# Kernel optimization log

Measured on AMD Instinct MI355X. Metric: run time of the kernel, lower is better.

## Reference

```python
import jax, jax.numpy as jnp
import numpy as np

B, D, IN_F, OUT_F, BLOCK = 2, 1024, 4096, 4096, 128
N_BLOCKS = IN_F // BLOCK  # 32


def setup_inputs() -> dict:
    key = jax.random.key(0)
    k1, k2, k3 = jax.random.split(key, 3)
    inputs = jax.random.normal(k1, (B, D, IN_F), dtype=jnp.float32)
    # int8 quantized weight buffer: [n_blocks, block_size, out_features]
    weight = jax.random.randint(k2, (N_BLOCKS, BLOCK, OUT_F), -128, 128, dtype=jnp.int32).astype(jnp.int8)
    # per-block, per-output-channel scaler: [n_blocks, out_features]
    weight_scaler = (jax.random.uniform(k3, (N_BLOCKS, OUT_F), dtype=jnp.float32) * 0.01 + 0.001)
    return {"inputs": inputs, "weight": weight, "weight_scaler": weight_scaler}


def reference(inputs, weight, weight_scaler):
    # Faithful port of WeightOnlyBlockwiseQuantizedLinear.blockwise_jax_kernel
    # (default path: symmetric quantization, zero_point is None).
    weight = weight.astype(jnp.int8)
    block_size = weight.shape[1]
    b, d, in_f = inputs.shape
    # [b, d, n_blocks s, block_size c]
    x = inputs.reshape(b, d, in_f // block_size, block_size)
    # per-block int8 matmul (promoted to float32 by x): [b, d, s, z]
    out = jnp.einsum("scz,bdsc->bdsz", weight, x)
    # apply per-block scaler and reduce over blocks: [b, d, z]
    out = jnp.einsum("bdsz,sz->bdz", out, weight_scaler)
    return out
```

## Files before the change

kernel.cpp:

```cpp
#include <hip/hip_runtime.h>
#include <hip/hip_bf16.h>


#define MDIM 2048
#define NDIM 4096
#define KDIM 4096
#define NBLK 32
#define BM 128
#define BN 128
#define BK 64

typedef __attribute__((ext_vector_type(8))) short bf16x8;
typedef __attribute__((ext_vector_type(4))) float f32x4;
typedef __attribute__((ext_vector_type(8))) unsigned short u16x8;

__device__ __forceinline__ unsigned short f2bf(float f) {
  unsigned u = __float_as_uint(f);
  u += 0x7fffu + ((u >> 16) & 1u);
  return (unsigned short)(u >> 16);
}

__device__ __forceinline__ void gl_lds16(const void* g, void* l) {
  __builtin_amdgcn_global_load_lds(
      (const __attribute__((address_space(1))) unsigned int*)g,
      (__attribute__((address_space(3))) unsigned int*)l,
      16, 0, 0);
}

__global__ void prep_a_kernel(const float* __restrict__ x,
                              unsigned short* __restrict__ ab) {
  int i = blockIdx.x * blockDim.x + threadIdx.x;
  const float4 v = reinterpret_cast<const float4*>(x)[i];
  ushort4 hv;
  hv.x = f2bf(v.x); hv.y = f2bf(v.y); hv.z = f2bf(v.z); hv.w = f2bf(v.w);
  reinterpret_cast<ushort4*>(ab)[i] = hv;
}

__global__ void prep_b_kernel(const int* __restrict__ w,
                              const float* __restrict__ scaler,
                              unsigned short* __restrict__ bt) {
  __shared__ __align__(16) unsigned short tile[64][72];
  const int t = threadIdx.x;
  const int k0 = blockIdx.y * 64;
  const int n0 = blockIdx.x * 64;
  const int s = k0 >> 7;
  {
    const int kl = t >> 2;
    const int nb = t & 3;
    const int nbase = n0 + nb * 16;
    const int4* src = reinterpret_cast<const int4*>(w + (size_t)(k0 + kl) * NDIM + nbase);
    const float4* scv = reinterpret_cast<const float4*>(scaler + (size_t)s * NDIM + nbase);
#pragma unroll
    for (int q = 0; q < 4; ++q) {
      const int4 v = src[q];
      const float4 sc = scv[q];
      tile[nb * 16 + q * 4 + 0][kl] = f2bf((float)v.x * sc.x);
      tile[nb * 16 + q * 4 + 1][kl] = f2bf((float)v.y * sc.y);
      tile[nb * 16 + q * 4 + 2][kl] = f2bf((float)v.z * sc.z);
      tile[nb * 16 + q * 4 + 3][kl] = f2bf((float)v.w * sc.w);
    }
  }
  __syncthreads();
  {
    const int nl = t >> 2;
#pragma unroll
    for (int q = 0; q < 2; ++q) {
      const int ch = (t & 3) * 2 + q;
      u16x8 v = *reinterpret_cast<const u16x8*>(&tile[nl][ch * 8]);
      *reinterpret_cast<u16x8*>(bt + (size_t)(n0 + nl) * KDIM + k0 + ch * 8) = v;
    }
  }
}

__global__ __launch_bounds__(256, 2)
void gemm_kernel(const unsigned short* __restrict__ ab,
                 const unsigned short* __restrict__ bt,
                 float* __restrict__ out) {
  __shared__ __align__(16) unsigned short lds_a[BM * BK];
  __shared__ __align__(16) unsigned short lds_b[BN * BK];

  const int t = threadIdx.x;
  const int lane = t & 63;
  const int wid = t >> 6;
  const int wm = wid >> 1;
  const int wn = wid & 1;
  const int lane15 = lane & 15;
  const int laneq = lane >> 4;
  const int swz = (lane & 7) << 4;

  const unsigned flat = blockIdx.x;
  const unsigned swzb = (flat & 7u) * 64u + (flat >> 3);
  const int ntile = swzb & 31;
  const int mtile = swzb >> 5;
  const int m0 = mtile * BM;
  const int n0 = ntile * BN;

  const int srow = t >> 3;
  const int sslot = (t & 7) ^ (srow & 7);
  const char* ga = (const char*)ab + ((size_t)(m0 + srow) * KDIM) * 2 + sslot * 16;
  const char* gb = (const char*)bt + ((size_t)(n0 + srow) * KDIM) * 2 + sslot * 16;
  const size_t rowstep = (size_t)32 * KDIM * 2;

  char* const la = (char*)lds_a;
  char* const lb = (char*)lds_b;
  const int ldst = wid * 8 * 128;

  int offA[4], offB[4];
#pragma unroll
  for (int i = 0; i < 4; ++i) {
    offA[i] = (wm * 64 + i * 16 + lane15) * 128 + laneq * 16;
    offB[i] = (wn * 64 + i * 16 + lane15) * 128 + laneq * 16;
  }

  const f32x4 fzero = {0.f, 0.f, 0.f, 0.f};
  f32x4 acc[4][4];
#pragma unroll
  for (int m = 0; m < 4; ++m)
#pragma unroll
    for (int n = 0; n < 4; ++n) acc[m][n] = fzero;

  for (int kt = 0; kt < KDIM / BK; ++kt) {
    const size_t koff = (size_t)kt * (BK * 2);
#pragma unroll
    for (int j = 0; j < 4; ++j) {
      gl_lds16(ga + koff + j * rowstep, la + ldst + j * 32 * 128);
      gl_lds16(gb + koff + j * rowstep, lb + ldst + j * 32 * 128);
    }
    __syncthreads();
#pragma unroll
    for (int tt = 0; tt < 2; ++tt) {
      bf16x8 af[4], bf[4];
#pragma unroll
      for (int i = 0; i < 4; ++i) {
        af[i] = *(const bf16x8*)(la + ((offA[i] + tt * 64) ^ swz));
        bf[i] = *(const bf16x8*)(lb + ((offB[i] + tt * 64) ^ swz));
      }
#pragma unroll
      for (int m = 0; m < 4; ++m)
#pragma unroll
        for (int n = 0; n < 4; ++n)
          acc[m][n] = __builtin_amdgcn_mfma_f32_16x16x32_bf16(af[m], bf[n], acc[m][n], 0, 0, 0);
    }
    __syncthreads();
  }

#pragma unroll
  for (int m = 0; m < 4; ++m)
#pragma unroll
    for (int r = 0; r < 4; ++r) {
      const int row = m0 + wm * 64 + m * 16 + laneq * 4 + r;
      float* op = out + (size_t)row * NDIM + n0 + wn * 64 + lane15;
#pragma unroll
      for (int n = 0; n < 4; ++n) op[n * 16] = acc[m][n][r];
    }
}

__global__ void fallback_kernel(const float* __restrict__ x,
                                const int* __restrict__ w,
                                const float* __restrict__ scaler,
                                float* __restrict__ out) {
  const int n = blockIdx.x * 256 + threadIdx.x;
  const int m = blockIdx.y;
  float acc = 0.f;
  for (int s = 0; s < NBLK; ++s) {
    float p = 0.f;
    const float* xr = x + (size_t)m * KDIM + s * 128;
    const int* wr = w + (size_t)s * 128 * NDIM + n;
#pragma unroll 8
    for (int c = 0; c < 128; ++c) p += xr[c] * (float)wr[(size_t)c * NDIM];
    acc += p * scaler[s * NDIM + n];
  }
  out[(size_t)m * NDIM + n] = acc;
}

extern "C" void kernel_launch(void* const* d_in, const int* in_sizes, int n_in,
                              void* d_out, int out_size, void* d_ws, size_t ws_size,
                              hipStream_t stream) {
  (void)in_sizes; (void)n_in; (void)out_size;
  const float* x = (const float*)d_in[0];
  const int* w = (const int*)d_in[1];
  const float* sc = (const float*)d_in[2];
  float* out = (float*)d_out;

  const size_t need = (size_t)51 * 1024 * 1024;
  if (ws_size >= need) {
    unsigned short* ab = (unsigned short*)d_ws;
    unsigned short* bt = ab + (size_t)MDIM * KDIM;
    prep_a_kernel<<<(MDIM * KDIM / 4) / 256, 256, 0, stream>>>(x, ab);
    prep_b_kernel<<<dim3(NDIM / 64, KDIM / 64), 256, 0, stream>>>(w, sc, bt);
    gemm_kernel<<<(MDIM / BM) * (NDIM / BN), 256, 0, stream>>>(ab, bt, out);
  } else {
    fallback_kernel<<<dim3(NDIM / 256, MDIM), 256, 0, stream>>>(x, w, sc, out);
  }
}
```

Baseline: 209.3 us.

## Double-buffer 128x256 GEMM tiles with 8 waves and ping-pong MFMA scheduling

Widens the GEMM tile to 128x256 with 512 threads and double-buffers the LDS stages, so global-to-LDS loads for step k+2 overlap MFMA work. The k-loop is split into quads of MFMAs separated by barriers with setprio, to interleave LDS reads and math across waves. The prep_b transpose tile gets an XOR swizzle to cut LDS bank conflicts. The larger LDS footprint lowers per-CU occupancy, and the many barriers add sync cost.

```diff
diff --git a/kernel.cpp b/kernel.cpp
--- a/kernel.cpp
+++ b/kernel.cpp
@@ -7,8 +7,9 @@
 #define KDIM 4096
 #define NBLK 32
 #define BM 128
-#define BN 128
+#define BN 256
 #define BK 64
+#define NT (KDIM / BK)
 
 typedef __attribute__((ext_vector_type(8))) short bf16x8;
 typedef __attribute__((ext_vector_type(4))) float f32x4;
@@ -54,44 +55,49 @@
     for (int q = 0; q < 4; ++q) {
       const int4 v = src[q];
       const float4 sc = scv[q];
-      tile[nb * 16 + q * 4 + 0][kl] = f2bf((float)v.x * sc.x);
-      tile[nb * 16 + q * 4 + 1][kl] = f2bf((float)v.y * sc.y);
-      tile[nb * 16 + q * 4 + 2][kl] = f2bf((float)v.z * sc.z);
-      tile[nb * 16 + q * 4 + 3][kl] = f2bf((float)v.w * sc.w);
+      const int rbase = nb * 16 + q * 4;
+      const int swzr = ((rbase >> 3) & 7) << 3;
+      const int ckl = kl ^ swzr;
+      tile[rbase + 0][ckl] = f2bf((float)v.x * sc.x);
+      tile[rbase + 1][ckl] = f2bf((float)v.y * sc.y);
+      tile[rbase + 2][ckl] = f2bf((float)v.z * sc.z);
+      tile[rbase + 3][ckl] = f2bf((float)v.w * sc.w);
     }
   }
   __syncthreads();
   {
     const int nl = t >> 2;
+    const int swzn = (nl >> 3) & 7;
 #pragma unroll
     for (int q = 0; q < 2; ++q) {
       const int ch = (t & 3) * 2 + q;
-      u16x8 v = *reinterpret_cast<const u16x8*>(&tile[nl][ch * 8]);
+      u16x8 v = *reinterpret_cast<const u16x8*>(&tile[nl][(ch ^ swzn) * 8]);
       *reinterpret_cast<u16x8*>(bt + (size_t)(n0 + nl) * KDIM + k0 + ch * 8) = v;
     }
   }
 }
 
-__global__ __launch_bounds__(256, 2)
+#define MFMA_BF16 __builtin_amdgcn_mfma_f32_16x16x32_bf16
+
+__global__ __launch_bounds__(512, 2)
 void gemm_kernel(const unsigned short* __restrict__ ab,
                  const unsigned short* __restrict__ bt,
                  float* __restrict__ out) {
-  __shared__ __align__(16) unsigned short lds_a[BM * BK];
-  __shared__ __align__(16) unsigned short lds_b[BN * BK];
+  __shared__ __align__(16) char lds[98304];
 
   const int t = threadIdx.x;
   const int lane = t & 63;
   const int wid = t >> 6;
-  const int wm = wid >> 1;
-  const int wn = wid & 1;
+  const int wm = wid >> 2;
+  const int wn = wid & 3;
   const int lane15 = lane & 15;
   const int laneq = lane >> 4;
   const int swz = (lane & 7) << 4;
 
   const unsigned flat = blockIdx.x;
-  const unsigned swzb = (flat & 7u) * 64u + (flat >> 3);
-  const int ntile = swzb & 31;
-  const int mtile = swzb >> 5;
+  const unsigned swzb = (flat & 7u) * 32u + (flat >> 3);
+  const int ntile = swzb & 15;
+  const int mtile = swzb >> 4;
   const int m0 = mtile * BM;
   const int n0 = ntile * BN;
 
@@ -99,11 +105,22 @@
   const int sslot = (t & 7) ^ (srow & 7);
   const char* ga = (const char*)ab + ((size_t)(m0 + srow) * KDIM) * 2 + sslot * 16;
   const char* gb = (const char*)bt + ((size_t)(n0 + srow) * KDIM) * 2 + sslot * 16;
-  const size_t rowstep = (size_t)32 * KDIM * 2;
-
-  char* const la = (char*)lds_a;
-  char* const lb = (char*)lds_b;
-  const int ldst = wid * 8 * 128;
+  const size_t rstep = (size_t)64 * KDIM * 2;
+
+  char* const lA0 = lds + (size_t)wid * 1024;
+  char* const lB0 = lds + 32768 + (size_t)wid * 1024;
+
+#define STAGE(kt, c) do {                                   \
+    const size_t ko_ = (size_t)(kt) * (BK * 2);             \
+    char* a_ = lA0 + (c) * 16384;                           \
+    char* b_ = lB0 + (c) * 32768;                           \
+    gl_lds16(ga + ko_,             a_);                     \
+    gl_lds16(ga + ko_ + rstep,     a_ + 8192);              \
+    gl_lds16(gb + ko_,             b_);                     \
+    gl_lds16(gb + ko_ + rstep,     b_ + 8192);              \
+    gl_lds16(gb + ko_ + 2 * rstep, b_ + 16384);             \
+    gl_lds16(gb + ko_ + 3 * rstep, b_ + 24576);             \
+  } while (0)
 
   int offA[4], offB[4];
 #pragma unroll
@@ -119,29 +136,63 @@
 #pragma unroll
     for (int n = 0; n < 4; ++n) acc[m][n] = fzero;
 
-  for (int kt = 0; kt < KDIM / BK; ++kt) {
-    const size_t koff = (size_t)kt * (BK * 2);
-#pragma unroll
-    for (int j = 0; j < 4; ++j) {
-      gl_lds16(ga + koff + j * rowstep, la + ldst + j * 32 * 128);
-      gl_lds16(gb + koff + j * rowstep, lb + ldst + j * 32 * 128);
-    }
-    __syncthreads();
-#pragma unroll
-    for (int tt = 0; tt < 2; ++tt) {
-      bf16x8 af[4], bf[4];
-#pragma unroll
-      for (int i = 0; i < 4; ++i) {
-        af[i] = *(const bf16x8*)(la + ((offA[i] + tt * 64) ^ swz));
-        bf[i] = *(const bf16x8*)(lb + ((offB[i] + tt * 64) ^ swz));
-      }
-#pragma unroll
-      for (int m = 0; m < 4; ++m)
-#pragma unroll
-        for (int n = 0; n < 4; ++n)
-          acc[m][n] = __builtin_amdgcn_mfma_f32_16x16x32_bf16(af[m], bf[n], acc[m][n], 0, 0, 0);
-    }
-    __syncthreads();
+  STAGE(0, 0);
+  STAGE(1, 1);
+  asm volatile("s_waitcnt vmcnt(6)" ::: "memory");
+  __builtin_amdgcn_s_barrier();
+
+#define LDA(m, base) do {                                             \
+    af[m][0] = *(const bf16x8*)((base) + ((offA[m]) ^ swz));          \
+    af[m][1] = *(const bf16x8*)((base) + ((offA[m] + 64) ^ swz));     \
+  } while (0)
+#define LDB(n, base) do {                                             \
+    bfr[n][0] = *(const bf16x8*)((base) + ((offB[n]) ^ swz));         \
+    bfr[n][1] = *(const bf16x8*)((base) + ((offB[n] + 64) ^ swz));    \
+  } while (0)
+#define QUAD(mA, mB, nA, nB) do {                                     \
+    __builtin_amdgcn_s_setprio(1);                                    \
+    acc[mA][nA] = MFMA_BF16(af[mA][0], bfr[nA][0], acc[mA][nA], 0, 0, 0); \
+    acc[mA][nB] = MFMA_BF16(af[mA][0], bfr[nB][0], acc[mA][nB], 0, 0, 0); \
+    acc[mB][nA] = MFMA_BF16(af[mB][0], bfr[nA][0], acc[mB][nA], 0, 0, 0); \
+    acc[mB][nB] = MFMA_BF16(af[mB][0], bfr[nB][0], acc[mB][nB], 0, 0, 0); \
+    acc[mA][nA] = MFMA_BF16(af[mA][1], bfr[nA][1], acc[mA][nA], 0, 0, 0); \
+    acc[mA][nB] = MFMA_BF16(af[mA][1], bfr[nB][1], acc[mA][nB], 0, 0, 0); \
+    acc[mB][nA] = MFMA_BF16(af[mB][1], bfr[nA][1], acc[mB][nA], 0, 0, 0); \
+    acc[mB][nB] = MFMA_BF16(af[mB][1], bfr[nB][1], acc[mB][nB], 0, 0, 0); \
+    __builtin_amdgcn_s_setprio(0);                                    \
+  } while (0)
+
+#pragma unroll 2
+  for (int t2 = 0; t2 < NT; ++t2) {
+    const int c = t2 & 1;
+    const char* lac = lds + c * 16384;
+    const char* lbc = lds + 32768 + c * 32768;
+    bf16x8 af[4][2], bfr[4][2];
+
+    LDA(0, lac); LDA(1, lac); LDB(0, lbc); LDB(1, lbc);
+    __builtin_amdgcn_s_barrier();
+    QUAD(0, 1, 0, 1);
+    __builtin_amdgcn_s_barrier();
+
+    LDB(2, lbc); LDB(3, lbc);
+    __builtin_amdgcn_s_barrier();
+    QUAD(0, 1, 2, 3);
+    __builtin_amdgcn_s_barrier();
+
+    LDA(2, lac); LDA(3, lac);
+    __builtin_amdgcn_s_barrier();
+    QUAD(2, 3, 2, 3);
+    __builtin_amdgcn_s_barrier();
+    __builtin_amdgcn_sched_barrier(0);
+
+    if (t2 + 2 < NT) STAGE(t2 + 2, c);
+    QUAD(2, 3, 0, 1);
+    if (t2 + 2 < NT) {
+      asm volatile("s_waitcnt vmcnt(6)" ::: "memory");
+    } else {
+      asm volatile("s_waitcnt vmcnt(0)" ::: "memory");
+    }
+    __builtin_amdgcn_s_barrier();
   }
 
 #pragma unroll
@@ -153,6 +204,10 @@
 #pragma unroll
       for (int n = 0; n < 4; ++n) op[n * 16] = acc[m][n][r];
     }
+#undef STAGE
+#undef LDA
+#undef LDB
+#undef QUAD
 }
 
 __global__ void fallback_kernel(const float* __restrict__ x,
@@ -188,7 +243,7 @@
     unsigned short* bt = ab + (size_t)MDIM * KDIM;
     prep_a_kernel<<<(MDIM * KDIM / 4) / 256, 256, 0, stream>>>(x, ab);
     prep_b_kernel<<<dim3(NDIM / 64, KDIM / 64), 256, 0, stream>>>(w, sc, bt);
-    gemm_kernel<<<(MDIM / BM) * (NDIM / BN), 256, 0, stream>>>(ab, bt, out);
+    gemm_kernel<<<(MDIM / BM) * (NDIM / BN), 512, 0, stream>>>(ab, bt, out);
   } else {
     fallback_kernel<<<dim3(NDIM / 256, MDIM), 256, 0, stream>>>(x, w, sc, out);
   }
```

Result: faster. 203.8 us (-2.6%).

## Fuse activation bf16 conversion into GEMM and rewrite weight prep without LDS

Applied to the files above, without the earlier changes.

Removes the separate prep_a kernel: the GEMM now loads fp32 activations directly, converts them to bf16 in registers with v_cvt_pk_bf16_f32, and writes them into swizzled LDS. The weight prep kernel is rewritten to transpose 8x8 sub-blocks in registers over 128x128 tiles, with no shared-memory tile. Occupancy hints are raised. This drops one launch and the round trip of the bf16 activation buffer through memory, but each GEMM tile now re-reads fp32 activations (twice the bytes) and converts them again, with synchronous loads in place of async global-to-LDS.

```diff
diff --git a/kernel.cpp b/kernel.cpp
--- a/kernel.cpp
+++ b/kernel.cpp
@@ -9,10 +9,12 @@
 #define BM 128
 #define BN 128
 #define BK 64
+#define NT (KDIM / BK)
 
 typedef __attribute__((ext_vector_type(8))) short bf16x8;
 typedef __attribute__((ext_vector_type(4))) float f32x4;
 typedef __attribute__((ext_vector_type(8))) unsigned short u16x8;
+typedef __attribute__((ext_vector_type(4))) unsigned int u32x4;
 
 __device__ __forceinline__ unsigned short f2bf(float f) {
   unsigned u = __float_as_uint(f);
@@ -27,57 +29,45 @@
       16, 0, 0);
 }
 
-__global__ void prep_a_kernel(const float* __restrict__ x,
-                              unsigned short* __restrict__ ab) {
-  int i = blockIdx.x * blockDim.x + threadIdx.x;
-  const float4 v = reinterpret_cast<const float4*>(x)[i];
-  ushort4 hv;
-  hv.x = f2bf(v.x); hv.y = f2bf(v.y); hv.z = f2bf(v.z); hv.w = f2bf(v.w);
-  reinterpret_cast<ushort4*>(ab)[i] = hv;
-}
-
-__global__ void prep_b_kernel(const int* __restrict__ w,
-                              const float* __restrict__ scaler,
-                              unsigned short* __restrict__ bt) {
-  __shared__ __align__(16) unsigned short tile[64][72];
+__global__ __launch_bounds__(256, 4)
+void prep_b_kernel(const int* __restrict__ w,
+                   const float* __restrict__ scaler,
+                   unsigned short* __restrict__ bt) {
   const int t = threadIdx.x;
-  const int k0 = blockIdx.y * 64;
-  const int n0 = blockIdx.x * 64;
-  const int s = k0 >> 7;
+  const int n0 = blockIdx.x * 128;
+  const int k0 = blockIdx.y * 128;
+  const int s = blockIdx.y;
+  const int k8 = (t & 15) * 8;
+  const int n8 = (t >> 4) * 8;
+
+  float sc[8];
   {
-    const int kl = t >> 2;
-    const int nb = t & 3;
-    const int nbase = n0 + nb * 16;
-    const int4* src = reinterpret_cast<const int4*>(w + (size_t)(k0 + kl) * NDIM + nbase);
-    const float4* scv = reinterpret_cast<const float4*>(scaler + (size_t)s * NDIM + nbase);
-#pragma unroll
-    for (int q = 0; q < 4; ++q) {
-      const int4 v = src[q];
-      const float4 sc = scv[q];
-      tile[nb * 16 + q * 4 + 0][kl] = f2bf((float)v.x * sc.x);
-      tile[nb * 16 + q * 4 + 1][kl] = f2bf((float)v.y * sc.y);
-      tile[nb * 16 + q * 4 + 2][kl] = f2bf((float)v.z * sc.z);
-      tile[nb * 16 + q * 4 + 3][kl] = f2bf((float)v.w * sc.w);
-    }
-  }
-  __syncthreads();
-  {
-    const int nl = t >> 2;
-#pragma unroll
-    for (int q = 0; q < 2; ++q) {
-      const int ch = (t & 3) * 2 + q;
-      u16x8 v = *reinterpret_cast<const u16x8*>(&tile[nl][ch * 8]);
-      *reinterpret_cast<u16x8*>(bt + (size_t)(n0 + nl) * KDIM + k0 + ch * 8) = v;
-    }
-  }
-}
-
-__global__ __launch_bounds__(256, 2)
-void gemm_kernel(const unsigned short* __restrict__ ab,
+    const float4* scv = reinterpret_cast<const float4*>(scaler + (size_t)s * NDIM + n0 + n8);
+    const float4 s0 = scv[0], s1 = scv[1];
+    sc[0] = s0.x; sc[1] = s0.y; sc[2] = s0.z; sc[3] = s0.w;
+    sc[4] = s1.x; sc[5] = s1.y; sc[6] = s1.z; sc[7] = s1.w;
+  }
+  u16x8 outv[8];
+#pragma unroll
+  for (int r = 0; r < 8; ++r) {
+    const int4* src = reinterpret_cast<const int4*>(w + (size_t)(k0 + k8 + r) * NDIM + n0 + n8);
+    const int4 a = src[0], b = src[1];
+    const int v[8] = {a.x, a.y, a.z, a.w, b.x, b.y, b.z, b.w};
+#pragma unroll
+    for (int j = 0; j < 8; ++j) outv[j][r] = f2bf((float)v[j] * sc[j]);
+  }
+#pragma unroll
+  for (int j = 0; j < 8; ++j)
+    *reinterpret_cast<u16x8*>(bt + (size_t)(n0 + n8 + j) * KDIM + k0 + k8) = outv[j];
+}
+
+#define MFMA_BF16 __builtin_amdgcn_mfma_f32_16x16x32_bf16
+
+__global__ __launch_bounds__(256, 3)
+void gemm_kernel(const float* __restrict__ x,
                  const unsigned short* __restrict__ bt,
                  float* __restrict__ out) {
-  __shared__ __align__(16) unsigned short lds_a[BM * BK];
-  __shared__ __align__(16) unsigned short lds_b[BN * BK];
+  __shared__ __align__(16) char lds[32768];
 
   const int t = threadIdx.x;
   const int lane = t & 63;
@@ -95,15 +85,23 @@
   const int m0 = mtile * BM;
   const int n0 = ntile * BN;
 
+  char* const lA = lds;
+  char* const lB = lds + 16384;
+
+  const int arow = t >> 3;
+  const int achk = t & 7;
+  const float* gx = x + (size_t)(m0 + arow) * KDIM + achk * 8;
+  const int aswz = (arow & 7) << 4;
+  int aoff[4];
+#pragma unroll
+  for (int p = 0; p < 4; ++p)
+    aoff[p] = (((arow + p * 32) * 128) + achk * 16) ^ aswz;
+
   const int srow = t >> 3;
   const int sslot = (t & 7) ^ (srow & 7);
-  const char* ga = (const char*)ab + ((size_t)(m0 + srow) * KDIM) * 2 + sslot * 16;
   const char* gb = (const char*)bt + ((size_t)(n0 + srow) * KDIM) * 2 + sslot * 16;
-  const size_t rowstep = (size_t)32 * KDIM * 2;
-
-  char* const la = (char*)lds_a;
-  char* const lb = (char*)lds_b;
-  const int ldst = wid * 8 * 128;
+  const size_t rstepB = (size_t)32 * KDIM * 2;
+  char* const lbst = lB + wid * 1024;
 
   int offA[4], offB[4];
 #pragma unroll
@@ -119,27 +117,44 @@
 #pragma unroll
     for (int n = 0; n < 4; ++n) acc[m][n] = fzero;
 
-  for (int kt = 0; kt < KDIM / BK; ++kt) {
-    const size_t koff = (size_t)kt * (BK * 2);
-#pragma unroll
-    for (int j = 0; j < 4; ++j) {
-      gl_lds16(ga + koff + j * rowstep, la + ldst + j * 32 * 128);
-      gl_lds16(gb + koff + j * rowstep, lb + ldst + j * 32 * 128);
-    }
+  for (int kt = 0; kt < NT; ++kt) {
+    float4 va[4][2];
+#pragma unroll
+    for (int p = 0; p < 4; ++p) {
+      const float* src = gx + (size_t)p * 32 * KDIM + kt * 64;
+      va[p][0] = *reinterpret_cast<const float4*>(src);
+      va[p][1] = *reinterpret_cast<const float4*>(src + 4);
+    }
+#pragma unroll
+    for (int p = 0; p < 4; ++p) {
+      unsigned d0, d1, d2, d3;
+      asm("v_cvt_pk_bf16_f32 %0, %1, %2" : "=v"(d0) : "v"(va[p][0].x), "v"(va[p][0].y));
+      asm("v_cvt_pk_bf16_f32 %0, %1, %2" : "=v"(d1) : "v"(va[p][0].z), "v"(va[p][0].w));
+      asm("v_cvt_pk_bf16_f32 %0, %1, %2" : "=v"(d2) : "v"(va[p][1].x), "v"(va[p][1].y));
+      asm("v_cvt_pk_bf16_f32 %0, %1, %2" : "=v"(d3) : "v"(va[p][1].z), "v"(va[p][1].w));
+      u32x4 wv = {d0, d1, d2, d3};
+      *reinterpret_cast<u32x4*>(lA + aoff[p]) = wv;
+    }
+    const size_t kob = (size_t)kt * (BK * 2);
+#pragma unroll
+    for (int j = 0; j < 4; ++j)
+      gl_lds16(gb + kob + j * rstepB, lbst + j * 4096);
+
     __syncthreads();
+
 #pragma unroll
     for (int tt = 0; tt < 2; ++tt) {
       bf16x8 af[4], bf[4];
 #pragma unroll
       for (int i = 0; i < 4; ++i) {
-        af[i] = *(const bf16x8*)(la + ((offA[i] + tt * 64) ^ swz));
-        bf[i] = *(const bf16x8*)(lb + ((offB[i] + tt * 64) ^ swz));
+        af[i] = *(const bf16x8*)(lA + ((offA[i] + tt * 64) ^ swz));
+        bf[i] = *(const bf16x8*)(lB + ((offB[i] + tt * 64) ^ swz));
       }
 #pragma unroll
       for (int m = 0; m < 4; ++m)
 #pragma unroll
         for (int n = 0; n < 4; ++n)
-          acc[m][n] = __builtin_amdgcn_mfma_f32_16x16x32_bf16(af[m], bf[n], acc[m][n], 0, 0, 0);
+          acc[m][n] = MFMA_BF16(af[m], bf[n], acc[m][n], 0, 0, 0);
     }
     __syncthreads();
   }
@@ -182,13 +197,11 @@
   const float* sc = (const float*)d_in[2];
   float* out = (float*)d_out;
 
-  const size_t need = (size_t)51 * 1024 * 1024;
+  const size_t need = (size_t)NDIM * KDIM * 2;
   if (ws_size >= need) {
-    unsigned short* ab = (unsigned short*)d_ws;
-    unsigned short* bt = ab + (size_t)MDIM * KDIM;
-    prep_a_kernel<<<(MDIM * KDIM / 4) / 256, 256, 0, stream>>>(x, ab);
-    prep_b_kernel<<<dim3(NDIM / 64, KDIM / 64), 256, 0, stream>>>(w, sc, bt);
-    gemm_kernel<<<(MDIM / BM) * (NDIM / BN), 256, 0, stream>>>(ab, bt, out);
+    unsigned short* bt = (unsigned short*)d_ws;
+    prep_b_kernel<<<dim3(NDIM / 128, KDIM / 128), 256, 0, stream>>>(w, sc, bt);
+    gemm_kernel<<<(MDIM / BM) * (NDIM / BN), 256, 0, stream>>>(x, bt, out);
   } else {
     fallback_kernel<<<dim3(NDIM / 256, MDIM), 256, 0, stream>>>(x, w, sc, out);
   }
```

Result: slower. 374.2 us (+78.8%).
